# Optimization experiments

Measured on AMD Instinct MI355X. Metric: run time of the kernel, lower is better.

Reference implementation:

```python
import jax, jax.numpy as jnp
import numpy as np

N_HEAD = 16
NEG = -1e30  # finite stand-in for -inf; keeps softmax NaN-free


def setup_inputs() -> dict:
    key = jax.random.key(0)
    k1, k2, k3, k4, k5, k6 = jax.random.split(key, 6)
    B, T, C = 4, 2048, 1024
    x = jax.random.normal(k1, (B, T, C), dtype=jnp.float32)
    # realistic right-padding: True = padded position
    lengths = jax.random.randint(k2, (B,), T // 2, T + 1)  # at least half valid
    padding_mask = jnp.arange(T)[None, :] >= lengths[:, None]  # [B,T] bool
    s = 0.02
    W_attn = jax.random.normal(k3, (C, 3 * C), dtype=jnp.float32) * s
    b_attn = jnp.zeros((3 * C,), dtype=jnp.float32)
    W_proj = jax.random.normal(k4, (C, C), dtype=jnp.float32) * s
    b_proj = jnp.zeros((C,), dtype=jnp.float32)
    return {"x": x, "padding_mask": padding_mask, "W_attn": W_attn,
            "b_attn": b_attn, "W_proj": W_proj, "b_proj": b_proj}


def reference(x, padding_mask, W_attn, b_attn, W_proj, b_proj):
    B, T, C = x.shape
    H, D = N_HEAD, C // N_HEAD
    qkv = x @ W_attn + b_attn  # [B,T,3C]
    q, k, v = jnp.split(qkv, 3, axis=-1)
    q = q.reshape(B, T, H, D).transpose(0, 2, 1, 3)  # [B,H,T,D]
    k = k.reshape(B, T, H, D).transpose(0, 2, 1, 3)
    v = v.reshape(B, T, H, D).transpose(0, 2, 1, 3)
    att = jnp.einsum('bhqd,bhkd->bhqk', q, k) / jnp.sqrt(jnp.float32(D))
    causal = jnp.tril(jnp.ones((T, T), dtype=bool))  # [T,T]
    invalid = padding_mask[:, None, None, :] | ~causal[None, None]  # [B,1,T,T] key invalid
    att = jnp.where(invalid, NEG, att)
    att = jax.nn.softmax(att, axis=-1)
    # rows where every key is masked: torch softmax gives NaN -> nan_to_num(0)
    any_valid = jnp.any(~invalid, axis=-1, keepdims=True)  # [B,1,T,1]
    att = jnp.where(any_valid, att, 0.0)
    y = jnp.einsum('bhqk,bhkd->bhqd', att, v)  # [B,H,T,D]
    y = y.transpose(0, 2, 1, 3).reshape(B, T, C)
    y = y @ W_proj + b_proj
    y = jnp.where(padding_mask[:, :, None], 0.0, y)
    return y
```

## Files before the change

### kernel.cpp

```cpp
#include <hip/hip_runtime.h>
#include <stdint.h>

#define T_SEQ 2048
#define CDIM  1024
#define NH    16
#define DH    64
#define BATCH 4
#define MROWS (BATCH * T_SEQ)
#define N3    (3 * CDIM)
#define NEGBIG -1e30f

typedef unsigned short u16;
typedef __attribute__((ext_vector_type(8))) __bf16 bf16x8;
typedef __attribute__((ext_vector_type(4))) __bf16 bf16x4;
typedef __attribute__((ext_vector_type(8))) unsigned short u16x8;
typedef __attribute__((ext_vector_type(4))) float f32x4;
typedef __attribute__((ext_vector_type(16))) float f32x16;
typedef __attribute__((ext_vector_type(4))) unsigned int u32x4;

__device__ inline u16 f2bf(float f) {
  uint32_t u = __builtin_bit_cast(uint32_t, f);
  u += 0x7FFFu + ((u >> 16) & 1u);
  return (u16)(u >> 16);
}

__device__ inline void gld_lds16(const void* g, void* l) {
  __builtin_amdgcn_global_load_lds(
      (const __attribute__((address_space(1))) void*)g,
      (__attribute__((address_space(3))) void*)l, 16, 0, 0);
}


__global__ __launch_bounds__(256) void cvt_f32_bf16(
    const float* __restrict__ in, u16* __restrict__ out, int n) {
  int i = (blockIdx.x * 256 + threadIdx.x) * 4;
  if (i >= n) return;
  float4 v = *(const float4*)&in[i];
  ushort4 o; o.x = f2bf(v.x); o.y = f2bf(v.y); o.z = f2bf(v.z); o.w = f2bf(v.w);
  *(ushort4*)&out[i] = o;
}

__global__ __launch_bounds__(256) void wt_tiled(
    const float* __restrict__ W, u16* __restrict__ WT, int K, int N) {
  __shared__ float tile[64][65];
  const int k0 = blockIdx.y * 64, n0 = blockIdx.x * 64;
  const int t = threadIdx.x, cr = t >> 6, cc = t & 63;
#pragma unroll
  for (int i = 0; i < 16; i++) {
    int r = i * 4 + cr;
    tile[r][cc] = W[(size_t)(k0 + r) * N + n0 + cc];
  }
  __syncthreads();
#pragma unroll
  for (int i = 0; i < 16; i++) {
    int r = i * 4 + cr;
    WT[(size_t)(n0 + r) * K + k0 + cc] = f2bf(tile[cc][r]);
  }
}

__global__ __launch_bounds__(256) void len_kernel(
    const void* __restrict__ maskp, int* __restrict__ lengths) {
  __shared__ int flag;
  __shared__ int red[256];
  const int t = threadIdx.x, b = blockIdx.x;
  if (t == 0) flag = 0;
  __syncthreads();
  const uint32_t* mw = (const uint32_t*)maskp;
  int f = 0;
  for (int i = t; i < 2048; i += 256) f |= (mw[i] > 1u) ? 1 : 0;
  if (f) atomicOr(&flag, 1);
  __syncthreads();
  int cnt = 0;
  if (flag) {
    const uint8_t* mb = (const uint8_t*)maskp;
    for (int i = t; i < T_SEQ; i += 256) cnt += (mb[(size_t)b * T_SEQ + i] == 0);
  } else {
    const int* mi = (const int*)maskp;
    for (int i = t; i < T_SEQ; i += 256) cnt += (mi[(size_t)b * T_SEQ + i] == 0);
  }
  red[t] = cnt;
  __syncthreads();
  for (int s = 128; s > 0; s >>= 1) {
    if (t < s) red[t] += red[t + s];
    __syncthreads();
  }
  if (t == 0) lengths[b] = red[0];
}

template <int MODE>
__global__ __launch_bounds__(256, 2) void gemm_bf16(
    const u16* __restrict__ A, const u16* __restrict__ Bt,
    const float* __restrict__ bias,
    u16* __restrict__ Qb, u16* __restrict__ Kb, u16* __restrict__ Vt,
    float* __restrict__ Out, const int* __restrict__ lengths,
    int Mdim, int Ndim, int Kdim) {
  __shared__ u16 SM[16384];
  u16* As = SM;
  u16* Bs = SM + 8192;
  const int t = threadIdx.x;
  const int lane = t & 63, wid = t >> 6;
  const int wr = wid >> 1, wc = wid & 1;
  const int r16 = lane & 15, kg = lane >> 4;
  const int m0 = blockIdx.y * 128, n0 = blockIdx.x * 128;

  f32x4 acc[4][4];
#pragma unroll
  for (int i = 0; i < 4; i++)
#pragma unroll
    for (int j = 0; j < 4; j++) acc[i][j] = (f32x4){0.f, 0.f, 0.f, 0.f};

  for (int k0 = 0; k0 < Kdim; k0 += 64) {
#pragma unroll
    for (int i = 0; i < 4; i++) {
      int idx = i * 256 + t;
      int row = idx >> 3;
      int chunk = idx & 7;
      int colel = (chunk * 8) ^ ((row & 7) << 3);
      gld_lds16(&A[(size_t)(m0 + row) * Kdim + k0 + colel], &As[idx * 8]);
      gld_lds16(&Bt[(size_t)(n0 + row) * Kdim + k0 + colel], &Bs[idx * 8]);
    }
    __syncthreads();

#pragma unroll
    for (int s = 0; s < 2; s++) {
      bf16x8 af[4], bfr[4];
#pragma unroll
      for (int m = 0; m < 4; m++) {
        int row = wr * 64 + m * 16 + r16;
        int colel = (s * 32 + kg * 8) ^ ((row & 7) << 3);
        af[m] = *(const bf16x8*)&As[row * 64 + colel];
      }
#pragma unroll
      for (int n = 0; n < 4; n++) {
        int row = wc * 64 + n * 16 + r16;
        int colel = (s * 32 + kg * 8) ^ ((row & 7) << 3);
        bfr[n] = *(const bf16x8*)&Bs[row * 64 + colel];
      }
#pragma unroll
      for (int m = 0; m < 4; m++)
#pragma unroll
        for (int n = 0; n < 4; n++)
          acc[m][n] = __builtin_amdgcn_mfma_f32_16x16x32_bf16(
              af[m], bfr[n], acc[m][n], 0, 0, 0);
    }
    __syncthreads();
  }

  if (MODE == 0 && n0 >= 2048) {
    u16* Tt = SM;
#pragma unroll
    for (int m = 0; m < 4; m++)
#pragma unroll
      for (int n = 0; n < 4; n++) {
        int ln = wc * 64 + n * 16 + r16;
        float bv = bias[n0 + ln];
#pragma unroll
        for (int reg = 0; reg < 4; reg++) {
          int lm = wr * 64 + m * 16 + kg * 4 + reg;
          Tt[ln * 128 + (lm ^ ((ln & 7) << 3))] = f2bf(acc[m][n][reg] + bv);
        }
      }
    __syncthreads();
    const int b = m0 >> 11;
    const int tt0 = m0 & 2047;
    const int cbase = n0 - 2048;
#pragma unroll
    for (int i = 0; i < 8; i++) {
      int u = i * 256 + t;
      int ln = u >> 4, ch = u & 15;
      u16x8 v = *(const u16x8*)&Tt[ln * 128 + ((ch * 8) ^ ((ln & 7) << 3))];
      int c = cbase + ln, hh = c >> 6, d = c & 63;
      *(u16x8*)&Vt[(((size_t)b * NH + hh) * DH + d) * T_SEQ + tt0 + ch * 8] = v;
    }
    return;
  }

#pragma unroll
  for (int m = 0; m < 4; m++) {
    int gmb = m0 + wr * 64 + m * 16 + kg * 4;
#pragma unroll
    for (int n = 0; n < 4; n++) {
      int gn = n0 + wc * 64 + n * 16 + r16;
      float bv = bias[gn];
#pragma unroll
      for (int reg = 0; reg < 4; reg++) {
        float v = acc[m][n][reg] + bv;
        int row = gmb + reg;
        int b = row >> 11, tt = row & 2047;
        if (MODE == 0) {
          int c = gn & 1023, h = c >> 6, d = c & 63;
          u16* dst = (gn < 1024) ? Qb : Kb;
          dst[((size_t)(b * NH + h) * T_SEQ + tt) * DH + d] = f2bf(v);
        } else {
          if (tt >= lengths[b]) v = 0.f;
          Out[(size_t)row * CDIM + gn] = v;
        }
      }
    }
  }
}

__global__ __launch_bounds__(256) void attn32_kernel(
    const u16* __restrict__ Qb, const u16* __restrict__ Kb,
    const u16* __restrict__ Vt, u16* __restrict__ yb,
    const int* __restrict__ lengths) {
  __shared__ __attribute__((aligned(16))) char smem[32768];
  const int t = threadIdx.x, lane = t & 63, wid = t >> 6;
  const int l31 = lane & 31, hi = lane >> 5;
  const int bh = blockIdx.y, b = bh >> 4, h = bh & (NH - 1);
  const int len = lengths[b];
  const int q0 = (int)(gridDim.x - 1 - blockIdx.x) * 128;
  if (q0 >= len) return;
  const int q0w = q0 + wid * 32;
  const int qrow = q0w + l31;
  const u16* Qh = Qb + (size_t)bh * T_SEQ * DH;
  const u16* Kh = Kb + (size_t)bh * T_SEQ * DH;
  const u16* Vth = Vt + (size_t)bh * DH * T_SEQ;

  bf16x8 qf[4];
#pragma unroll
  for (int ks = 0; ks < 4; ks++)
    qf[ks] = *(const bf16x8*)&Qh[(size_t)qrow * DH + ks * 16 + hi * 8];

  f32x16 oacc[2];
  oacc[0] = (f32x16)0.f; oacc[1] = (f32x16)0.f;
  float mrun = NEGBIG, lrun = 0.f;
  const float SC = 0.18033688011112042f;

  const int lenceil = (len + 63) & ~63;
  const int kv_end = (q0 + 128 < lenceil) ? q0 + 128 : lenceil;
  const int ntiles = kv_end >> 6;

  const int idx0 = t, idx1 = 256 + t;
  const int row0 = idx0 >> 3, ch0 = idx0 & 7;
  const int row1 = idx1 >> 3, ch1 = idx1 & 7;
  const int kc0 = (ch0 * 8) ^ ((row0 & 7) << 3);
  const int kc1 = (ch1 * 8) ^ ((row1 & 7) << 3);
  const char* kp0 = (const char*)Kh + ((size_t)row0 * DH + kc0) * 2;
  const char* kp1 = (const char*)Kh + ((size_t)row1 * DH + kc1) * 2;
  const char* vp0 = (const char*)Vth + ((size_t)row0 * T_SEQ + kc0) * 2;
  const char* vp1 = (const char*)Vth + ((size_t)row1 * T_SEQ + kc1) * 2;

  auto STAGE = [&](int bufsel) {
    char* base = smem + bufsel * 16384;
    gld_lds16(kp0, base + idx0 * 16);
    gld_lds16(kp1, base + idx1 * 16);
    gld_lds16(vp0, base + 8192 + idx0 * 16);
    gld_lds16(vp1, base + 8192 + idx1 * 16);
    kp0 += 8192; kp1 += 8192; vp0 += 128; vp1 += 128;
  };

  STAGE(0);
  __syncthreads();
  int cur = 0;

  for (int it = 0; it < ntiles; ++it) {
    const int kv0 = it << 6;
    if (it + 1 < ntiles) STAGE(cur ^ 1);
    const u16* Ks = (const u16*)(smem + cur * 16384);
    const u16* Vts = (const u16*)(smem + cur * 16384 + 8192);

    if (kv0 <= q0w + 31) {
      f32x16 sacc[2];
      sacc[0] = (f32x16)0.f; sacc[1] = (f32x16)0.f;
#pragma unroll
      for (int kb = 0; kb < 2; kb++)
#pragma unroll
        for (int ks = 0; ks < 4; ks++) {
          int row = kb * 32 + l31;
          int col = (ks * 16 + hi * 8) ^ ((row & 7) << 3);
          bf16x8 ak = *(const bf16x8*)&Ks[row * 64 + col];
          sacc[kb] = __builtin_amdgcn_mfma_f32_32x32x16_bf16(
              ak, qf[ks], sacc[kb], 0, 0, 0);
        }

      const bool need_mask = (kv0 + 63 > q0w) || (kv0 + 64 > len);
#pragma unroll
      for (int kb = 0; kb < 2; kb++)
#pragma unroll
        for (int r = 0; r < 16; r++) {
          float s2 = sacc[kb][r] * SC;
          if (need_mask) {
            int key = kv0 + kb * 32 + (r & 3) + 8 * (r >> 2) + 4 * hi;
            if (key > qrow || key >= len) s2 = NEGBIG;
          }
          sacc[kb][r] = s2;
        }

      float tm[16];
#pragma unroll
      for (int r = 0; r < 16; r++) tm[r] = fmaxf(sacc[0][r], sacc[1][r]);
#pragma unroll
      for (int r = 0; r < 8; r++) tm[r] = fmaxf(tm[r], tm[r + 8]);
#pragma unroll
      for (int r = 0; r < 4; r++) tm[r] = fmaxf(tm[r], tm[r + 4]);
      tm[0] = fmaxf(fmaxf(tm[0], tm[2]), fmaxf(tm[1], tm[3]));
      float mt = fmaxf(tm[0], __shfl_xor(tm[0], 32));

      if (!__all(mt <= mrun + 8.f)) {
        float mnew = fmaxf(mrun, mt);
        float fac = exp2f(mrun - mnew);
        mrun = mnew;
        lrun *= fac;
#pragma unroll
        for (int r = 0; r < 16; r++) { oacc[0][r] *= fac; oacc[1][r] *= fac; }
      }

#pragma unroll
      for (int kb = 0; kb < 2; kb++)
#pragma unroll
        for (int r = 0; r < 16; r++) sacc[kb][r] = exp2f(sacc[kb][r] - mrun);
      float pt[16];
#pragma unroll
      for (int r = 0; r < 16; r++) pt[r] = sacc[0][r] + sacc[1][r];
#pragma unroll
      for (int r = 0; r < 8; r++) pt[r] += pt[r + 8];
#pragma unroll
      for (int r = 0; r < 4; r++) pt[r] += pt[r + 4];
      float ps = (pt[0] + pt[2]) + (pt[1] + pt[3]);
      ps += __shfl_xor(ps, 32);
      lrun += ps;

#pragma unroll
      for (int ks = 0; ks < 4; ks++) {
        const int kb = ks >> 1, rb = (ks & 1) * 8;
        uint32_t d0, d1, d2, d3;
        asm("v_cvt_pk_bf16_f32 %0, %1, %2" : "=v"(d0)
            : "v"(sacc[kb][rb + 0]), "v"(sacc[kb][rb + 1]));
        asm("v_cvt_pk_bf16_f32 %0, %1, %2" : "=v"(d1)
            : "v"(sacc[kb][rb + 2]), "v"(sacc[kb][rb + 3]));
        asm("v_cvt_pk_bf16_f32 %0, %1, %2" : "=v"(d2)
            : "v"(sacc[kb][rb + 4]), "v"(sacc[kb][rb + 5]));
        asm("v_cvt_pk_bf16_f32 %0, %1, %2" : "=v"(d3)
            : "v"(sacc[kb][rb + 6]), "v"(sacc[kb][rb + 7]));
        bf16x8 pb = __builtin_bit_cast(bf16x8, (u32x4){d0, d1, d2, d3});
#pragma unroll
        for (int mb = 0; mb < 2; mb++) {
          int row = mb * 32 + l31;
          int sw = (row & 7);
          bf16x4 v1 = *(const bf16x4*)&Vts[row * 64 + ((2 * ks) ^ sw) * 8 + 4 * hi];
          bf16x4 v2 = *(const bf16x4*)&Vts[row * 64 + ((2 * ks + 1) ^ sw) * 8 + 4 * hi];
          bf16x8 av;
#pragma unroll
          for (int j = 0; j < 4; j++) { av[j] = v1[j]; av[4 + j] = v2[j]; }
          oacc[mb] = __builtin_amdgcn_mfma_f32_32x32x16_bf16(
              av, pb, oacc[mb], 0, 0, 0);
        }
      }
    }
    __syncthreads();
    cur ^= 1;
  }

  const float inv = (lrun > 0.f) ? 1.f / lrun : 0.f;
  u16* yt = (u16*)smem + wid * (32 * 72);
#pragma unroll
  for (int mb = 0; mb < 2; mb++)
#pragma unroll
    for (int r = 0; r < 16; r += 2) {
      int d = mb * 32 + (r & 3) + 8 * (r >> 2) + 4 * hi;
      float a0 = oacc[mb][r] * inv, a1 = oacc[mb][r + 1] * inv;
      uint32_t pw;
      asm("v_cvt_pk_bf16_f32 %0, %1, %2" : "=v"(pw) : "v"(a0), "v"(a1));
      *(uint32_t*)&yt[l31 * 72 + d] = pw;
    }
  asm volatile("s_waitcnt lgkmcnt(0)" ::: "memory");
#pragma unroll
  for (int pass = 0; pass < 4; pass++) {
    int rowq = pass * 8 + (lane >> 3);
    int col8 = (lane & 7) * 8;
    u16x8 v = *(const u16x8*)&yt[rowq * 72 + col8];
    *(u16x8*)&yb[((size_t)b * T_SEQ + q0w + rowq) * CDIM + h * DH + col8] = v;
  }
}

extern "C" void kernel_launch(void* const* d_in, const int* in_sizes, int n_in,
                              void* d_out, int out_size, void* d_ws, size_t ws_size,
                              hipStream_t stream) {
  const float* x  = (const float*)d_in[0];
  const void*  mask = d_in[1];
  const float* Wa = (const float*)d_in[2];
  const float* ba = (const float*)d_in[3];
  const float* Wp = (const float*)d_in[4];
  const float* bp = (const float*)d_in[5];
  float* out = (float*)d_out;

  char* w = (char*)d_ws;
  u16* xb  = (u16*)w; w += (size_t)MROWS * CDIM * 2;
  u16* WaT = (u16*)w; w += (size_t)N3 * CDIM * 2;
  u16* WpT = (u16*)w; w += (size_t)CDIM * CDIM * 2;
  u16* Qb  = (u16*)w; w += (size_t)MROWS * CDIM * 2;
  u16* Kb  = (u16*)w; w += (size_t)MROWS * CDIM * 2;
  u16* Vt  = (u16*)w; w += (size_t)MROWS * CDIM * 2;
  int* lengths = (int*)w;
  u16* yb = xb;

  cvt_f32_bf16<<<(MROWS * CDIM / 4 + 255) / 256, 256, 0, stream>>>(x, xb, MROWS * CDIM);
  wt_tiled<<<dim3(N3 / 64, CDIM / 64), 256, 0, stream>>>(Wa, WaT, CDIM, N3);
  wt_tiled<<<dim3(CDIM / 64, CDIM / 64), 256, 0, stream>>>(Wp, WpT, CDIM, CDIM);
  len_kernel<<<BATCH, 256, 0, stream>>>(mask, lengths);

  gemm_bf16<0><<<dim3(N3 / 128, MROWS / 128), 256, 0, stream>>>(
      xb, WaT, ba, Qb, Kb, Vt, nullptr, nullptr, MROWS, N3, CDIM);

  attn32_kernel<<<dim3(T_SEQ / 128, BATCH * NH), 256, 0, stream>>>(
      Qb, Kb, Vt, yb, lengths);

  gemm_bf16<1><<<dim3(CDIM / 128, MROWS / 128), 256, 0, stream>>>(
      yb, WpT, bp, nullptr, nullptr, nullptr, out, lengths, MROWS, CDIM, CDIM);
}
```

Baseline: 257.7 us.

## Pair low/high causal query tiles per block sharing K/V loads with 4-stage pipeline

Each attention block now handles two 128-row query tiles, one near the start of the sequence and one mirrored near the end. Both share the same staged K/V tiles from LDS, which balances causal work across blocks and halves the grid. The LDS ring grows to four 16KB buffers with two tiles prefetched ahead, using explicit vmcnt waits and a raw barrier instead of __syncthreads. It also folds the scale into the exp via fma, raises the lazy-rescale threshold, and adds s_setprio around the MFMAs; the cost is more registers and fewer blocks, which may reduce occupancy.

After: 244.5 us. 5.1% less time.

```diff
diff --git a/kernel.cpp b/kernel.cpp
--- a/kernel.cpp
+++ b/kernel.cpp
@@ -200,36 +200,43 @@
   }
 }
 
-__global__ __launch_bounds__(256) void attn32_kernel(
+__global__ __launch_bounds__(256) void attn32p_kernel(
     const u16* __restrict__ Qb, const u16* __restrict__ Kb,
     const u16* __restrict__ Vt, u16* __restrict__ yb,
     const int* __restrict__ lengths) {
-  __shared__ __attribute__((aligned(16))) char smem[32768];
+  __shared__ __attribute__((aligned(16))) char smem[65536];
   const int t = threadIdx.x, lane = t & 63, wid = t >> 6;
   const int l31 = lane & 31, hi = lane >> 5;
   const int bh = blockIdx.y, b = bh >> 4, h = bh & (NH - 1);
   const int len = lengths[b];
-  const int q0 = (int)(gridDim.x - 1 - blockIdx.x) * 128;
-  if (q0 >= len) return;
-  const int q0w = q0 + wid * 32;
-  const int qrow = q0w + l31;
+  const int iq = blockIdx.x;
+  const int q0L = iq * 128;
+  const int q0H = (15 - iq) * 128;
+  const bool hiAct = q0H < len;
+  const int q0Lw = q0L + wid * 32, q0Hw = q0H + wid * 32;
+  const int qrowL = q0Lw + l31, qrowH = q0Hw + l31;
   const u16* Qh = Qb + (size_t)bh * T_SEQ * DH;
   const u16* Kh = Kb + (size_t)bh * T_SEQ * DH;
   const u16* Vth = Vt + (size_t)bh * DH * T_SEQ;
-
-  bf16x8 qf[4];
-#pragma unroll
-  for (int ks = 0; ks < 4; ks++)
-    qf[ks] = *(const bf16x8*)&Qh[(size_t)qrow * DH + ks * 16 + hi * 8];
-
-  f32x16 oacc[2];
-  oacc[0] = (f32x16)0.f; oacc[1] = (f32x16)0.f;
-  float mrun = NEGBIG, lrun = 0.f;
   const float SC = 0.18033688011112042f;
+  const float THR = 44.3614195558365f;
 
   const int lenceil = (len + 63) & ~63;
-  const int kv_end = (q0 + 128 < lenceil) ? q0 + 128 : lenceil;
+  const int kvH = (q0H + 128 < lenceil) ? q0H + 128 : lenceil;
+  const int kv_end = hiAct ? kvH : (q0L + 128);
   const int ntiles = kv_end >> 6;
+
+  bf16x8 qfL[4], qfH[4];
+#pragma unroll
+  for (int ks = 0; ks < 4; ks++) {
+    qfL[ks] = *(const bf16x8*)&Qh[(size_t)qrowL * DH + ks * 16 + hi * 8];
+    qfH[ks] = *(const bf16x8*)&Qh[(size_t)qrowH * DH + ks * 16 + hi * 8];
+  }
+
+  f32x16 oaccL[2], oaccH[2];
+  oaccL[0] = (f32x16)0.f; oaccL[1] = (f32x16)0.f;
+  oaccH[0] = (f32x16)0.f; oaccH[1] = (f32x16)0.f;
+  float mL = NEGBIG, lL = 0.f, mH = NEGBIG, lH = 0.f;
 
   const int idx0 = t, idx1 = 256 + t;
   const int row0 = idx0 >> 3, ch0 = idx0 & 7;
@@ -241,8 +248,8 @@
   const char* vp0 = (const char*)Vth + ((size_t)row0 * T_SEQ + kc0) * 2;
   const char* vp1 = (const char*)Vth + ((size_t)row1 * T_SEQ + kc1) * 2;
 
-  auto STAGE = [&](int bufsel) {
-    char* base = smem + bufsel * 16384;
+  auto STAGE = [&](int bsel) {
+    char* base = smem + bsel * 16384;
     gld_lds16(kp0, base + idx0 * 16);
     gld_lds16(kp1, base + idx1 * 16);
     gld_lds16(vp0, base + 8192 + idx0 * 16);
@@ -250,128 +257,144 @@
     kp0 += 8192; kp1 += 8192; vp0 += 128; vp1 += 128;
   };
 
-  STAGE(0);
+  auto FLASH = [&](const u16* Ks, const u16* Vts, int kv0, int q0w, int qrow,
+                   bf16x8* qf, f32x16* oacc, float& mrun, float& lrun) {
+    f32x16 sacc[2];
+    sacc[0] = (f32x16)0.f; sacc[1] = (f32x16)0.f;
+    __builtin_amdgcn_s_setprio(1);
+#pragma unroll
+    for (int kb = 0; kb < 2; kb++)
+#pragma unroll
+      for (int ks = 0; ks < 4; ks++) {
+        int row = kb * 32 + l31;
+        int col = (ks * 16 + hi * 8) ^ ((row & 7) << 3);
+        bf16x8 ak = *(const bf16x8*)&Ks[row * 64 + col];
+        sacc[kb] = __builtin_amdgcn_mfma_f32_32x32x16_bf16(
+            ak, qf[ks], sacc[kb], 0, 0, 0);
+      }
+    __builtin_amdgcn_s_setprio(0);
+
+    if ((kv0 + 63 > q0w) || (kv0 + 64 > len)) {
+#pragma unroll
+      for (int kb = 0; kb < 2; kb++)
+#pragma unroll
+        for (int r = 0; r < 16; r++) {
+          int key = kv0 + kb * 32 + (r & 3) + 8 * (r >> 2) + 4 * hi;
+          if (key > qrow || key >= len) sacc[kb][r] = NEGBIG;
+        }
+    }
+    float tm[16];
+#pragma unroll
+    for (int r = 0; r < 16; r++) tm[r] = fmaxf(sacc[0][r], sacc[1][r]);
+#pragma unroll
+    for (int r = 0; r < 8; r++) tm[r] = fmaxf(tm[r], tm[r + 8]);
+#pragma unroll
+    for (int r = 0; r < 4; r++) tm[r] = fmaxf(tm[r], tm[r + 4]);
+    tm[0] = fmaxf(fmaxf(tm[0], tm[2]), fmaxf(tm[1], tm[3]));
+    float mt = fmaxf(tm[0], __shfl_xor(tm[0], 32));
+
+    if (!__all(mt <= mrun + THR)) {
+      float mnew = fmaxf(mrun, mt);
+      float fac = exp2f((mrun - mnew) * SC);
+      mrun = mnew;
+      lrun *= fac;
+#pragma unroll
+      for (int r = 0; r < 16; r++) { oacc[0][r] *= fac; oacc[1][r] *= fac; }
+    }
+    const float msc = mrun * SC;
+#pragma unroll
+    for (int kb = 0; kb < 2; kb++)
+#pragma unroll
+      for (int r = 0; r < 16; r++)
+        sacc[kb][r] = exp2f(fmaf(sacc[kb][r], SC, -msc));
+    float pt[16];
+#pragma unroll
+    for (int r = 0; r < 16; r++) pt[r] = sacc[0][r] + sacc[1][r];
+#pragma unroll
+    for (int r = 0; r < 8; r++) pt[r] += pt[r + 8];
+#pragma unroll
+    for (int r = 0; r < 4; r++) pt[r] += pt[r + 4];
+    float ps = (pt[0] + pt[2]) + (pt[1] + pt[3]);
+    ps += __shfl_xor(ps, 32);
+    lrun += ps;
+
+#pragma unroll
+    for (int ks = 0; ks < 4; ks++) {
+      const int kb = ks >> 1, rb = (ks & 1) * 8;
+      uint32_t d0, d1, d2, d3;
+      asm("v_cvt_pk_bf16_f32 %0, %1, %2" : "=v"(d0)
+          : "v"(sacc[kb][rb + 0]), "v"(sacc[kb][rb + 1]));
+      asm("v_cvt_pk_bf16_f32 %0, %1, %2" : "=v"(d1)
+          : "v"(sacc[kb][rb + 2]), "v"(sacc[kb][rb + 3]));
+      asm("v_cvt_pk_bf16_f32 %0, %1, %2" : "=v"(d2)
+          : "v"(sacc[kb][rb + 4]), "v"(sacc[kb][rb + 5]));
+      asm("v_cvt_pk_bf16_f32 %0, %1, %2" : "=v"(d3)
+          : "v"(sacc[kb][rb + 6]), "v"(sacc[kb][rb + 7]));
+      bf16x8 pb = __builtin_bit_cast(bf16x8, (u32x4){d0, d1, d2, d3});
+      __builtin_amdgcn_s_setprio(1);
+#pragma unroll
+      for (int mb = 0; mb < 2; mb++) {
+        int row = mb * 32 + l31;
+        int sw = (row & 7);
+        bf16x4 v1 = *(const bf16x4*)&Vts[row * 64 + ((2 * ks) ^ sw) * 8 + 4 * hi];
+        bf16x4 v2 = *(const bf16x4*)&Vts[row * 64 + ((2 * ks + 1) ^ sw) * 8 + 4 * hi];
+        bf16x8 av;
+#pragma unroll
+        for (int j = 0; j < 4; j++) { av[j] = v1[j]; av[4 + j] = v2[j]; }
+        oacc[mb] = __builtin_amdgcn_mfma_f32_32x32x16_bf16(
+            av, pb, oacc[mb], 0, 0, 0);
+      }
+      __builtin_amdgcn_s_setprio(0);
+    }
+  };
+
+  STAGE(0); STAGE(1);
+  for (int it = 0; it < ntiles; ++it) {
+    if (it + 2 < ntiles) STAGE((it + 2) & 3);
+    const int r = ntiles - 1 - it;
+    if (r >= 2)      asm volatile("s_waitcnt vmcnt(8)" ::: "memory");
+    else if (r == 1) asm volatile("s_waitcnt vmcnt(4)" ::: "memory");
+    else             asm volatile("s_waitcnt vmcnt(0)" ::: "memory");
+    __builtin_amdgcn_s_barrier();
+    __builtin_amdgcn_sched_barrier(0);
+
+    const u16* Ks  = (const u16*)(smem + (it & 3) * 16384);
+    const u16* Vts = (const u16*)(smem + (it & 3) * 16384 + 8192);
+    const int kv0 = it << 6;
+    if (hiAct && kv0 <= q0Hw + 31)
+      FLASH(Ks, Vts, kv0, q0Hw, qrowH, qfH, oaccH, mH, lH);
+    if (kv0 <= q0Lw + 31)
+      FLASH(Ks, Vts, kv0, q0Lw, qrowL, qfL, oaccL, mL, lL);
+  }
   __syncthreads();
-  int cur = 0;
-
-  for (int it = 0; it < ntiles; ++it) {
-    const int kv0 = it << 6;
-    if (it + 1 < ntiles) STAGE(cur ^ 1);
-    const u16* Ks = (const u16*)(smem + cur * 16384);
-    const u16* Vts = (const u16*)(smem + cur * 16384 + 8192);
-
-    if (kv0 <= q0w + 31) {
-      f32x16 sacc[2];
-      sacc[0] = (f32x16)0.f; sacc[1] = (f32x16)0.f;
-#pragma unroll
-      for (int kb = 0; kb < 2; kb++)
-#pragma unroll
-        for (int ks = 0; ks < 4; ks++) {
-          int row = kb * 32 + l31;
-          int col = (ks * 16 + hi * 8) ^ ((row & 7) << 3);
-          bf16x8 ak = *(const bf16x8*)&Ks[row * 64 + col];
-          sacc[kb] = __builtin_amdgcn_mfma_f32_32x32x16_bf16(
-              ak, qf[ks], sacc[kb], 0, 0, 0);
-        }
-
-      const bool need_mask = (kv0 + 63 > q0w) || (kv0 + 64 > len);
-#pragma unroll
-      for (int kb = 0; kb < 2; kb++)
-#pragma unroll
-        for (int r = 0; r < 16; r++) {
-          float s2 = sacc[kb][r] * SC;
-          if (need_mask) {
-            int key = kv0 + kb * 32 + (r & 3) + 8 * (r >> 2) + 4 * hi;
-            if (key > qrow || key >= len) s2 = NEGBIG;
-          }
-          sacc[kb][r] = s2;
-        }
-
-      float tm[16];
-#pragma unroll
-      for (int r = 0; r < 16; r++) tm[r] = fmaxf(sacc[0][r], sacc[1][r]);
-#pragma unroll
-      for (int r = 0; r < 8; r++) tm[r] = fmaxf(tm[r], tm[r + 8]);
-#pragma unroll
-      for (int r = 0; r < 4; r++) tm[r] = fmaxf(tm[r], tm[r + 4]);
-      tm[0] = fmaxf(fmaxf(tm[0], tm[2]), fmaxf(tm[1], tm[3]));
-      float mt = fmaxf(tm[0], __shfl_xor(tm[0], 32));
-
-      if (!__all(mt <= mrun + 8.f)) {
-        float mnew = fmaxf(mrun, mt);
-        float fac = exp2f(mrun - mnew);
-        mrun = mnew;
-        lrun *= fac;
-#pragma unroll
-        for (int r = 0; r < 16; r++) { oacc[0][r] *= fac; oacc[1][r] *= fac; }
-      }
-
-#pragma unroll
-      for (int kb = 0; kb < 2; kb++)
-#pragma unroll
-        for (int r = 0; r < 16; r++) sacc[kb][r] = exp2f(sacc[kb][r] - mrun);
-      float pt[16];
-#pragma unroll
-      for (int r = 0; r < 16; r++) pt[r] = sacc[0][r] + sacc[1][r];
-#pragma unroll
-      for (int r = 0; r < 8; r++) pt[r] += pt[r + 8];
-#pragma unroll
-      for (int r = 0; r < 4; r++) pt[r] += pt[r + 4];
-      float ps = (pt[0] + pt[2]) + (pt[1] + pt[3]);
-      ps += __shfl_xor(ps, 32);
-      lrun += ps;
-
-#pragma unroll
-      for (int ks = 0; ks < 4; ks++) {
-        const int kb = ks >> 1, rb = (ks & 1) * 8;
-        uint32_t d0, d1, d2, d3;
-        asm("v_cvt_pk_bf16_f32 %0, %1, %2" : "=v"(d0)
-            : "v"(sacc[kb][rb + 0]), "v"(sacc[kb][rb + 1]));
-        asm("v_cvt_pk_bf16_f32 %0, %1, %2" : "=v"(d1)
-            : "v"(sacc[kb][rb + 2]), "v"(sacc[kb][rb + 3]));
-        asm("v_cvt_pk_bf16_f32 %0, %1, %2" : "=v"(d2)
-            : "v"(sacc[kb][rb + 4]), "v"(sacc[kb][rb + 5]));
-        asm("v_cvt_pk_bf16_f32 %0, %1, %2" : "=v"(d3)
-            : "v"(sacc[kb][rb + 6]), "v"(sacc[kb][rb + 7]));
-        bf16x8 pb = __builtin_bit_cast(bf16x8, (u32x4){d0, d1, d2, d3});
-#pragma unroll
-        for (int mb = 0; mb < 2; mb++) {
-          int row = mb * 32 + l31;
-          int sw = (row & 7);
-          bf16x4 v1 = *(const bf16x4*)&Vts[row * 64 + ((2 * ks) ^ sw) * 8 + 4 * hi];
-          bf16x4 v2 = *(const bf16x4*)&Vts[row * 64 + ((2 * ks + 1) ^ sw) * 8 + 4 * hi];
-          bf16x8 av;
-#pragma unroll
-          for (int j = 0; j < 4; j++) { av[j] = v1[j]; av[4 + j] = v2[j]; }
-          oacc[mb] = __builtin_amdgcn_mfma_f32_32x32x16_bf16(
-              av, pb, oacc[mb], 0, 0, 0);
-        }
-      }
-    }
-    __syncthreads();
-    cur ^= 1;
-  }
-
-  const float inv = (lrun > 0.f) ? 1.f / lrun : 0.f;
+
   u16* yt = (u16*)smem + wid * (32 * 72);
-#pragma unroll
-  for (int mb = 0; mb < 2; mb++)
-#pragma unroll
-    for (int r = 0; r < 16; r += 2) {
-      int d = mb * 32 + (r & 3) + 8 * (r >> 2) + 4 * hi;
-      float a0 = oacc[mb][r] * inv, a1 = oacc[mb][r + 1] * inv;
-      uint32_t pw;
-      asm("v_cvt_pk_bf16_f32 %0, %1, %2" : "=v"(pw) : "v"(a0), "v"(a1));
-      *(uint32_t*)&yt[l31 * 72 + d] = pw;
-    }
-  asm volatile("s_waitcnt lgkmcnt(0)" ::: "memory");
-#pragma unroll
-  for (int pass = 0; pass < 4; pass++) {
-    int rowq = pass * 8 + (lane >> 3);
-    int col8 = (lane & 7) * 8;
-    u16x8 v = *(const u16x8*)&yt[rowq * 72 + col8];
-    *(u16x8*)&yb[((size_t)b * T_SEQ + q0w + rowq) * CDIM + h * DH + col8] = v;
-  }
+  auto EPI = [&](f32x16* oacc, float lrun, int q0w) {
+    const float inv = (lrun > 0.f) ? 1.f / lrun : 0.f;
+#pragma unroll
+    for (int mb = 0; mb < 2; mb++)
+#pragma unroll
+      for (int r = 0; r < 16; r += 2) {
+        int d = mb * 32 + (r & 3) + 8 * (r >> 2) + 4 * hi;
+        float a0 = oacc[mb][r] * inv, a1 = oacc[mb][r + 1] * inv;
+        uint32_t pw;
+        asm("v_cvt_pk_bf16_f32 %0, %1, %2" : "=v"(pw) : "v"(a0), "v"(a1));
+        *(uint32_t*)&yt[l31 * 72 + d] = pw;
+      }
+    asm volatile("s_waitcnt lgkmcnt(0)" ::: "memory");
+    __builtin_amdgcn_sched_barrier(0);
+#pragma unroll
+    for (int pass = 0; pass < 4; pass++) {
+      int rowq = pass * 8 + (lane >> 3);
+      int col8 = (lane & 7) * 8;
+      u16x8 v = *(const u16x8*)&yt[rowq * 72 + col8];
+      *(u16x8*)&yb[((size_t)b * T_SEQ + q0w + rowq) * CDIM + h * DH + col8] = v;
+    }
+    asm volatile("s_waitcnt lgkmcnt(0)" ::: "memory");
+    __builtin_amdgcn_sched_barrier(0);
+  };
+  EPI(oaccL, lL, q0Lw);
+  if (hiAct) EPI(oaccH, lH, q0Hw);
 }
 
 extern "C" void kernel_launch(void* const* d_in, const int* in_sizes, int n_in,
@@ -403,7 +426,7 @@
   gemm_bf16<0><<<dim3(N3 / 128, MROWS / 128), 256, 0, stream>>>(
       xb, WaT, ba, Qb, Kb, Vt, nullptr, nullptr, MROWS, N3, CDIM);
 
-  attn32_kernel<<<dim3(T_SEQ / 128, BATCH * NH), 256, 0, stream>>>(
+  attn32p_kernel<<<dim3(8, BATCH * NH), 256, 0, stream>>>(
       Qb, Kb, Vt, yb, lengths);
 
   gemm_bf16<1><<<dim3(CDIM / 128, MROWS / 128), 256, 0, stream>>>(
```

## Pair causal query tiles per block and map heads to XCDs in attention

Applied to the files above, without the earlier changes.

The attention kernel now launches a 1D grid where each block handles a low 64-row query tile and its mirrored high tile, so causal work per block is balanced. Block IDs are remapped so all tiles of one batch-head land on the same XCD, which should improve L2 reuse of K/V. It also folds the softmax scale into an FMA inside exp2 with a scaled rescale threshold, adds s_setprio around MFMA sections, and reorders barrier/prefetch. In exchange, waves in the low pair sit idle through the extra KV tiles loaded for the high tile.

New measurement: 242.4 us. 1.06x faster.

```diff
diff --git a/kernel.cpp b/kernel.cpp
--- a/kernel.cpp
+++ b/kernel.cpp
@@ -200,22 +200,37 @@
   }
 }
 
-__global__ __launch_bounds__(256) void attn32_kernel(
+__global__ __launch_bounds__(256) void attn32p_kernel(
     const u16* __restrict__ Qb, const u16* __restrict__ Kb,
     const u16* __restrict__ Vt, u16* __restrict__ yb,
     const int* __restrict__ lengths) {
   __shared__ __attribute__((aligned(16))) char smem[32768];
   const int t = threadIdx.x, lane = t & 63, wid = t >> 6;
   const int l31 = lane & 31, hi = lane >> 5;
-  const int bh = blockIdx.y, b = bh >> 4, h = bh & (NH - 1);
+  const int wgid = blockIdx.x;
+  const int xcd = wgid & 7, slot = wgid >> 3;
+  const int bh = xcd * 8 + (slot >> 4);
+  const int iq = slot & 15;
+  const int b = bh >> 4, h = bh & (NH - 1);
   const int len = lengths[b];
-  const int q0 = (int)(gridDim.x - 1 - blockIdx.x) * 128;
-  if (q0 >= len) return;
-  const int q0w = q0 + wid * 32;
+  const int n64 = (len + 63) >> 6;
+  const int npairs = (n64 + 1) >> 1;
+  if (iq >= npairs) return;
+  const int q0L = iq * 64;
+  const int q0H = (n64 - 1 - iq) * 64;
+  const bool hiAct = q0H > q0L;
+  const int wp = wid >> 1, w2 = wid & 1;
+  const bool act = (wp == 0) || hiAct;
+  const int q0w = (wp ? q0H : q0L) + w2 * 32;
   const int qrow = q0w + l31;
   const u16* Qh = Qb + (size_t)bh * T_SEQ * DH;
   const u16* Kh = Kb + (size_t)bh * T_SEQ * DH;
   const u16* Vth = Vt + (size_t)bh * DH * T_SEQ;
+  const float SC = 0.18033688011112042f;
+  const float THR = 44.3614195558365f;
+
+  const int kv_end = (hiAct ? q0H : q0L) + 64;
+  const int ntiles = kv_end >> 6;
 
   bf16x8 qf[4];
 #pragma unroll
@@ -225,11 +240,6 @@
   f32x16 oacc[2];
   oacc[0] = (f32x16)0.f; oacc[1] = (f32x16)0.f;
   float mrun = NEGBIG, lrun = 0.f;
-  const float SC = 0.18033688011112042f;
-
-  const int lenceil = (len + 63) & ~63;
-  const int kv_end = (q0 + 128 < lenceil) ? q0 + 128 : lenceil;
-  const int ntiles = kv_end >> 6;
 
   const int idx0 = t, idx1 = 256 + t;
   const int row0 = idx0 >> 3, ch0 = idx0 & 7;
@@ -241,8 +251,8 @@
   const char* vp0 = (const char*)Vth + ((size_t)row0 * T_SEQ + kc0) * 2;
   const char* vp1 = (const char*)Vth + ((size_t)row1 * T_SEQ + kc1) * 2;
 
-  auto STAGE = [&](int bufsel) {
-    char* base = smem + bufsel * 16384;
+  auto STAGE = [&](int bsel) {
+    char* base = smem + bsel * 16384;
     gld_lds16(kp0, base + idx0 * 16);
     gld_lds16(kp1, base + idx1 * 16);
     gld_lds16(vp0, base + 8192 + idx0 * 16);
@@ -250,127 +260,132 @@
     kp0 += 8192; kp1 += 8192; vp0 += 128; vp1 += 128;
   };
 
+  auto FLASH = [&](const u16* Ks, const u16* Vts, int kv0) {
+    f32x16 sacc[2];
+    sacc[0] = (f32x16)0.f; sacc[1] = (f32x16)0.f;
+    __builtin_amdgcn_s_setprio(1);
+#pragma unroll
+    for (int kb = 0; kb < 2; kb++)
+#pragma unroll
+      for (int ks = 0; ks < 4; ks++) {
+        int row = kb * 32 + l31;
+        int col = (ks * 16 + hi * 8) ^ ((row & 7) << 3);
+        bf16x8 ak = *(const bf16x8*)&Ks[row * 64 + col];
+        sacc[kb] = __builtin_amdgcn_mfma_f32_32x32x16_bf16(
+            ak, qf[ks], sacc[kb], 0, 0, 0);
+      }
+    __builtin_amdgcn_s_setprio(0);
+
+    if ((kv0 + 63 > q0w) || (kv0 + 64 > len)) {
+#pragma unroll
+      for (int kb = 0; kb < 2; kb++)
+#pragma unroll
+        for (int r = 0; r < 16; r++) {
+          int key = kv0 + kb * 32 + (r & 3) + 8 * (r >> 2) + 4 * hi;
+          if (key > qrow || key >= len) sacc[kb][r] = NEGBIG;
+        }
+    }
+    float tm[16];
+#pragma unroll
+    for (int r = 0; r < 16; r++) tm[r] = fmaxf(sacc[0][r], sacc[1][r]);
+#pragma unroll
+    for (int r = 0; r < 8; r++) tm[r] = fmaxf(tm[r], tm[r + 8]);
+#pragma unroll
+    for (int r = 0; r < 4; r++) tm[r] = fmaxf(tm[r], tm[r + 4]);
+    tm[0] = fmaxf(fmaxf(tm[0], tm[2]), fmaxf(tm[1], tm[3]));
+    float mt = fmaxf(tm[0], __shfl_xor(tm[0], 32));
+
+    if (!__all(mt <= mrun + THR)) {
+      float mnew = fmaxf(mrun, mt);
+      float fac = exp2f((mrun - mnew) * SC);
+      mrun = mnew;
+      lrun *= fac;
+#pragma unroll
+      for (int r = 0; r < 16; r++) { oacc[0][r] *= fac; oacc[1][r] *= fac; }
+    }
+    const float msc = mrun * SC;
+#pragma unroll
+    for (int kb = 0; kb < 2; kb++)
+#pragma unroll
+      for (int r = 0; r < 16; r++)
+        sacc[kb][r] = exp2f(fmaf(sacc[kb][r], SC, -msc));
+    float pt[16];
+#pragma unroll
+    for (int r = 0; r < 16; r++) pt[r] = sacc[0][r] + sacc[1][r];
+#pragma unroll
+    for (int r = 0; r < 8; r++) pt[r] += pt[r + 8];
+#pragma unroll
+    for (int r = 0; r < 4; r++) pt[r] += pt[r + 4];
+    float ps = (pt[0] + pt[2]) + (pt[1] + pt[3]);
+    ps += __shfl_xor(ps, 32);
+    lrun += ps;
+
+#pragma unroll
+    for (int ks = 0; ks < 4; ks++) {
+      const int kb = ks >> 1, rb = (ks & 1) * 8;
+      uint32_t d0, d1, d2, d3;
+      asm("v_cvt_pk_bf16_f32 %0, %1, %2" : "=v"(d0)
+          : "v"(sacc[kb][rb + 0]), "v"(sacc[kb][rb + 1]));
+      asm("v_cvt_pk_bf16_f32 %0, %1, %2" : "=v"(d1)
+          : "v"(sacc[kb][rb + 2]), "v"(sacc[kb][rb + 3]));
+      asm("v_cvt_pk_bf16_f32 %0, %1, %2" : "=v"(d2)
+          : "v"(sacc[kb][rb + 4]), "v"(sacc[kb][rb + 5]));
+      asm("v_cvt_pk_bf16_f32 %0, %1, %2" : "=v"(d3)
+          : "v"(sacc[kb][rb + 6]), "v"(sacc[kb][rb + 7]));
+      bf16x8 pb = __builtin_bit_cast(bf16x8, (u32x4){d0, d1, d2, d3});
+      __builtin_amdgcn_s_setprio(1);
+#pragma unroll
+      for (int mb = 0; mb < 2; mb++) {
+        int row = mb * 32 + l31;
+        int sw = (row & 7);
+        bf16x4 v1 = *(const bf16x4*)&Vts[row * 64 + ((2 * ks) ^ sw) * 8 + 4 * hi];
+        bf16x4 v2 = *(const bf16x4*)&Vts[row * 64 + ((2 * ks + 1) ^ sw) * 8 + 4 * hi];
+        bf16x8 av;
+#pragma unroll
+        for (int j = 0; j < 4; j++) { av[j] = v1[j]; av[4 + j] = v2[j]; }
+        oacc[mb] = __builtin_amdgcn_mfma_f32_32x32x16_bf16(
+            av, pb, oacc[mb], 0, 0, 0);
+      }
+      __builtin_amdgcn_s_setprio(0);
+    }
+  };
+
   STAGE(0);
+  for (int it = 0; it < ntiles; ++it) {
+    asm volatile("s_waitcnt vmcnt(0)" ::: "memory");
+    __builtin_amdgcn_s_barrier();
+    __builtin_amdgcn_sched_barrier(0);
+    if (it + 1 < ntiles) STAGE((it + 1) & 1);
+
+    const u16* Ks  = (const u16*)(smem + (it & 1) * 16384);
+    const u16* Vts = (const u16*)(smem + (it & 1) * 16384 + 8192);
+    const int kv0 = it << 6;
+    if (act && kv0 <= q0w + 31) FLASH(Ks, Vts, kv0);
+  }
   __syncthreads();
-  int cur = 0;
-
-  for (int it = 0; it < ntiles; ++it) {
-    const int kv0 = it << 6;
-    if (it + 1 < ntiles) STAGE(cur ^ 1);
-    const u16* Ks = (const u16*)(smem + cur * 16384);
-    const u16* Vts = (const u16*)(smem + cur * 16384 + 8192);
-
-    if (kv0 <= q0w + 31) {
-      f32x16 sacc[2];
-      sacc[0] = (f32x16)0.f; sacc[1] = (f32x16)0.f;
-#pragma unroll
-      for (int kb = 0; kb < 2; kb++)
-#pragma unroll
-        for (int ks = 0; ks < 4; ks++) {
-          int row = kb * 32 + l31;
-          int col = (ks * 16 + hi * 8) ^ ((row & 7) << 3);
-          bf16x8 ak = *(const bf16x8*)&Ks[row * 64 + col];
-          sacc[kb] = __builtin_amdgcn_mfma_f32_32x32x16_bf16(
-              ak, qf[ks], sacc[kb], 0, 0, 0);
-        }
-
-      const bool need_mask = (kv0 + 63 > q0w) || (kv0 + 64 > len);
-#pragma unroll
-      for (int kb = 0; kb < 2; kb++)
-#pragma unroll
-        for (int r = 0; r < 16; r++) {
-          float s2 = sacc[kb][r] * SC;
-          if (need_mask) {
-            int key = kv0 + kb * 32 + (r & 3) + 8 * (r >> 2) + 4 * hi;
-            if (key > qrow || key >= len) s2 = NEGBIG;
-          }
-          sacc[kb][r] = s2;
-        }
-
-      float tm[16];
-#pragma unroll
-      for (int r = 0; r < 16; r++) tm[r] = fmaxf(sacc[0][r], sacc[1][r]);
-#pragma unroll
-      for (int r = 0; r < 8; r++) tm[r] = fmaxf(tm[r], tm[r + 8]);
-#pragma unroll
-      for (int r = 0; r < 4; r++) tm[r] = fmaxf(tm[r], tm[r + 4]);
-      tm[0] = fmaxf(fmaxf(tm[0], tm[2]), fmaxf(tm[1], tm[3]));
-      float mt = fmaxf(tm[0], __shfl_xor(tm[0], 32));
-
-      if (!__all(mt <= mrun + 8.f)) {
-        float mnew = fmaxf(mrun, mt);
-        float fac = exp2f(mrun - mnew);
-        mrun = mnew;
-        lrun *= fac;
-#pragma unroll
-        for (int r = 0; r < 16; r++) { oacc[0][r] *= fac; oacc[1][r] *= fac; }
-      }
-
-#pragma unroll
-      for (int kb = 0; kb < 2; kb++)
-#pragma unroll
-        for (int r = 0; r < 16; r++) sacc[kb][r] = exp2f(sacc[kb][r] - mrun);
-      float pt[16];
-#pragma unroll
-      for (int r = 0; r < 16; r++) pt[r] = sacc[0][r] + sacc[1][r];
-#pragma unroll
-      for (int r = 0; r < 8; r++) pt[r] += pt[r + 8];
-#pragma unroll
-      for (int r = 0; r < 4; r++) pt[r] += pt[r + 4];
-      float ps = (pt[0] + pt[2]) + (pt[1] + pt[3]);
-      ps += __shfl_xor(ps, 32);
-      lrun += ps;
-
-#pragma unroll
-      for (int ks = 0; ks < 4; ks++) {
-        const int kb = ks >> 1, rb = (ks & 1) * 8;
-        uint32_t d0, d1, d2, d3;
-        asm("v_cvt_pk_bf16_f32 %0, %1, %2" : "=v"(d0)
-            : "v"(sacc[kb][rb + 0]), "v"(sacc[kb][rb + 1]));
-        asm("v_cvt_pk_bf16_f32 %0, %1, %2" : "=v"(d1)
-            : "v"(sacc[kb][rb + 2]), "v"(sacc[kb][rb + 3]));
-        asm("v_cvt_pk_bf16_f32 %0, %1, %2" : "=v"(d2)
-            : "v"(sacc[kb][rb + 4]), "v"(sacc[kb][rb + 5]));
-        asm("v_cvt_pk_bf16_f32 %0, %1, %2" : "=v"(d3)
-            : "v"(sacc[kb][rb + 6]), "v"(sacc[kb][rb + 7]));
-        bf16x8 pb = __builtin_bit_cast(bf16x8, (u32x4){d0, d1, d2, d3});
-#pragma unroll
-        for (int mb = 0; mb < 2; mb++) {
-          int row = mb * 32 + l31;
-          int sw = (row & 7);
-          bf16x4 v1 = *(const bf16x4*)&Vts[row * 64 + ((2 * ks) ^ sw) * 8 + 4 * hi];
-          bf16x4 v2 = *(const bf16x4*)&Vts[row * 64 + ((2 * ks + 1) ^ sw) * 8 + 4 * hi];
-          bf16x8 av;
-#pragma unroll
-          for (int j = 0; j < 4; j++) { av[j] = v1[j]; av[4 + j] = v2[j]; }
-          oacc[mb] = __builtin_amdgcn_mfma_f32_32x32x16_bf16(
-              av, pb, oacc[mb], 0, 0, 0);
-        }
-      }
-    }
-    __syncthreads();
-    cur ^= 1;
-  }
-
-  const float inv = (lrun > 0.f) ? 1.f / lrun : 0.f;
-  u16* yt = (u16*)smem + wid * (32 * 72);
-#pragma unroll
-  for (int mb = 0; mb < 2; mb++)
-#pragma unroll
-    for (int r = 0; r < 16; r += 2) {
-      int d = mb * 32 + (r & 3) + 8 * (r >> 2) + 4 * hi;
-      float a0 = oacc[mb][r] * inv, a1 = oacc[mb][r + 1] * inv;
-      uint32_t pw;
-      asm("v_cvt_pk_bf16_f32 %0, %1, %2" : "=v"(pw) : "v"(a0), "v"(a1));
-      *(uint32_t*)&yt[l31 * 72 + d] = pw;
-    }
-  asm volatile("s_waitcnt lgkmcnt(0)" ::: "memory");
-#pragma unroll
-  for (int pass = 0; pass < 4; pass++) {
-    int rowq = pass * 8 + (lane >> 3);
-    int col8 = (lane & 7) * 8;
-    u16x8 v = *(const u16x8*)&yt[rowq * 72 + col8];
-    *(u16x8*)&yb[((size_t)b * T_SEQ + q0w + rowq) * CDIM + h * DH + col8] = v;
+
+  if (act) {
+    u16* yt = (u16*)smem + wid * (32 * 72);
+    const float inv = (lrun > 0.f) ? 1.f / lrun : 0.f;
+#pragma unroll
+    for (int mb = 0; mb < 2; mb++)
+#pragma unroll
+      for (int r = 0; r < 16; r += 2) {
+        int d = mb * 32 + (r & 3) + 8 * (r >> 2) + 4 * hi;
+        float a0 = oacc[mb][r] * inv, a1 = oacc[mb][r + 1] * inv;
+        uint32_t pw;
+        asm("v_cvt_pk_bf16_f32 %0, %1, %2" : "=v"(pw) : "v"(a0), "v"(a1));
+        *(uint32_t*)&yt[l31 * 72 + d] = pw;
+      }
+    asm volatile("s_waitcnt lgkmcnt(0)" ::: "memory");
+    __builtin_amdgcn_sched_barrier(0);
+#pragma unroll
+    for (int pass = 0; pass < 4; pass++) {
+      int rowq = pass * 8 + (lane >> 3);
+      int col8 = (lane & 7) * 8;
+      u16x8 v = *(const u16x8*)&yt[rowq * 72 + col8];
+      *(u16x8*)&yb[((size_t)b * T_SEQ + q0w + rowq) * CDIM + h * DH + col8] = v;
+    }
   }
 }
 
@@ -403,7 +418,7 @@
   gemm_bf16<0><<<dim3(N3 / 128, MROWS / 128), 256, 0, stream>>>(
       xb, WaT, ba, Qb, Kb, Vt, nullptr, nullptr, MROWS, N3, CDIM);
 
-  attn32_kernel<<<dim3(T_SEQ / 128, BATCH * NH), 256, 0, stream>>>(
+  attn32p_kernel<<<dim3(1024), 256, 0, stream>>>(
       Qb, Kb, Vt, yb, lengths);
 
   gemm_bf16<1><<<dim3(CDIM / 128, MROWS / 128), 256, 0, stream>>>(
```
